# Performance work log

Measured on AMD Instinct MI355X. Metric: run time of the kernel, lower is better.

The kernel has to match this reference:

```python
import jax, jax.numpy as jnp
import numpy as np

N = 4096
M0 = 2048
M1 = 2048
MCS = 4096
STRIDE = 2
D_NNGP = STRIDE ** 2 * M1              # 8192, input dim of layer-1 arccos maps
D_NTK = STRIDE ** 2 * (MCS + M1)       # 24576, input dim1 of layer-1 count sketch


def setup_inputs() -> dict:
    key = jax.random.key(0)
    ks = jax.random.split(key, 8)
    return {
        "layer_idx": 1,
        "z_nngp": jax.random.normal(ks[0], (N, D_NNGP), jnp.float32),
        "z_ntk": jax.random.normal(ks[1], (N, D_NTK), jnp.float32),
        "W0": jax.random.normal(ks[2], (D_NNGP, M0), jnp.float32),   # arccos0[1].W
        "W1": jax.random.normal(ks[3], (D_NNGP, M1), jnp.float32),   # arccos1[1].W
        "sign1": (jax.random.randint(ks[4], (D_NTK,), 0, 2) * 2 - 1).astype(jnp.float32),
        "indx1": jax.random.randint(ks[5], (D_NTK,), 0, MCS),
        "sign2": (jax.random.randint(ks[6], (M0,), 0, 2) * 2 - 1).astype(jnp.float32),
        "indx2": jax.random.randint(ks[7], (M0,), 0, MCS),
    }


def count_sketch(x, indx, sign, out_dim):
    # x: [n, d_in]; sign-multiply then scatter_add along last axis into out_dim bins
    xs = x * sign[None, :]
    out = jnp.zeros((x.shape[0], out_dim), dtype=x.dtype)
    return out.at[:, indx].add(xs)


def reference(layer_idx, z_nngp, z_ntk, W0, W1, sign1, indx1, sign2, indx2):
    norm0 = np.sqrt(2.0 / M0).astype(np.float32)
    norm1 = np.float32(np.sqrt(2.0 / M1) / 2.0)
    # arccos order-0 feature map (step function)
    xw0 = z_nngp @ W0
    tmp = (xw0 > 0).astype(z_nngp.dtype) * norm0          # [N, M0]
    # arccos order-1 feature map (relu-like: |xw| + xw)
    xw1 = z_nngp @ W1
    z_nngp_out = (jnp.abs(xw1) + xw1) * norm1             # [N, M1]
    # tensor sketch: count-sketch both, FFT, complex pointwise multiply, ifft.real
    x_cs = count_sketch(z_ntk, indx1, sign1, MCS)         # [N, MCS]
    y_cs = count_sketch(tmp, indx2, sign2, MCS)           # [N, MCS]
    z_ntk_out = jnp.fft.ifft(jnp.fft.fft(x_cs, axis=-1) * jnp.fft.fft(y_cs, axis=-1)).real
    z_ntk_cat = jnp.concatenate([z_nngp_out, z_ntk_out], axis=1)  # [N, M1+MCS]
    return (z_nngp_out, z_ntk_cat)
```

## Files before the change

kernel.cpp:

```cpp
#include <hip/hip_runtime.h>

#define NROW 4096
#define KDIM 8192
#define MDIM 2048
#define MCS_ 4096
#define DNTK 24576
#define CATW 6144
#define TAU_HALF 2.5e-3f
#define NT (KDIM / 32)

typedef __attribute__((ext_vector_type(8))) short short8;
typedef __attribute__((ext_vector_type(4))) float f32x4;

__device__ __forceinline__ void split2(float x0, float x1,
                                       unsigned& hi, unsigned& lo) {
    const unsigned u0 = __float_as_uint(x0);
    const unsigned u1 = __float_as_uint(x1);
    hi = (u0 >> 16) | (u1 & 0xFFFF0000u);
    const float l0 = x0 - __uint_as_float(u0 & 0xFFFF0000u);
    const float l1 = x1 - __uint_as_float(u1 & 0xFFFF0000u);
    lo = (__float_as_uint(l0) >> 16) | (__float_as_uint(l1) & 0xFFFF0000u);
}

__device__ __forceinline__ float2 cmulf(float2 a, float2 b) {
    return make_float2(a.x * b.x - a.y * b.y, a.x * b.y + a.y * b.x);
}

__global__ __launch_bounds__(512, 2) void gemm_mfma(
    const float* __restrict__ A,
    const float* __restrict__ W1,
    const float* __restrict__ W0,
    float* __restrict__ out0,
    float* __restrict__ outCat)
{
    const int mode = blockIdx.z;
    const float* __restrict__ W = mode ? W0 : W1;

    __shared__ short8 AhiS[2][1024], AloS[2][1024];
    __shared__ short8 BhiS[2][1024], BloS[2][1024];

    const int tid  = threadIdx.x;
    const int lane = tid & 63;
    const int wid  = tid >> 6;
    const int wr   = wid >> 1;
    const int wc   = wid & 1;
    const int brow = blockIdx.y * 256;
    const int bcol = blockIdx.x * 256;

    f32x4 acc[4][8];
#pragma unroll
    for (int m = 0; m < 4; ++m)
#pragma unroll
        for (int n = 0; n < 8; ++n)
#pragma unroll
            for (int i = 0; i < 4; ++i) acc[m][n][i] = 0.f;

    const int srow  = tid >> 1;
    const int skh   = tid & 1;
    const int slot0 = (srow >> 4) * 64 + (srow & 15) + (skh << 5);
    const float* aptr = A + (size_t)(brow + srow) * KDIM + skh * 16;
    const float* bptr = W + (size_t)(skh * 16) * MDIM + (bcol + srow);

    float4 av0, av1, av2, av3;
    float  bst[16];

#define LOAD_TILE(T)                                                         \
    {                                                                        \
        const float* ap = aptr + (T) * 32;                                   \
        av0 = *reinterpret_cast<const float4*>(ap);                          \
        av1 = *reinterpret_cast<const float4*>(ap + 4);                      \
        av2 = *reinterpret_cast<const float4*>(ap + 8);                      \
        av3 = *reinterpret_cast<const float4*>(ap + 12);                     \
        const float* bp = bptr + (size_t)((T) * 32) * MDIM;                  \
        _Pragma("unroll")                                                    \
        for (int j = 0; j < 16; ++j) bst[j] = bp[(size_t)j * MDIM];          \
    }

#define CONVERT_WRITE(BUF)                                                   \
    {                                                                        \
        union { short8 s; unsigned u[4]; } h, l;                             \
        split2(av0.x, av0.y, h.u[0], l.u[0]);                                \
        split2(av0.z, av0.w, h.u[1], l.u[1]);                                \
        split2(av1.x, av1.y, h.u[2], l.u[2]);                                \
        split2(av1.z, av1.w, h.u[3], l.u[3]);                                \
        AhiS[BUF][slot0] = h.s;  AloS[BUF][slot0] = l.s;                     \
        split2(av2.x, av2.y, h.u[0], l.u[0]);                                \
        split2(av2.z, av2.w, h.u[1], l.u[1]);                                \
        split2(av3.x, av3.y, h.u[2], l.u[2]);                                \
        split2(av3.z, av3.w, h.u[3], l.u[3]);                                \
        AhiS[BUF][slot0 + 16] = h.s;  AloS[BUF][slot0 + 16] = l.s;           \
        split2(bst[0], bst[1], h.u[0], l.u[0]);                              \
        split2(bst[2], bst[3], h.u[1], l.u[1]);                              \
        split2(bst[4], bst[5], h.u[2], l.u[2]);                              \
        split2(bst[6], bst[7], h.u[3], l.u[3]);                              \
        BhiS[BUF][slot0] = h.s;  BloS[BUF][slot0] = l.s;                     \
        split2(bst[8],  bst[9],  h.u[0], l.u[0]);                            \
        split2(bst[10], bst[11], h.u[1], l.u[1]);                            \
        split2(bst[12], bst[13], h.u[2], l.u[2]);                            \
        split2(bst[14], bst[15], h.u[3], l.u[3]);                            \
        BhiS[BUF][slot0 + 16] = h.s;  BloS[BUF][slot0 + 16] = l.s;           \
    }

    LOAD_TILE(0);
    CONVERT_WRITE(0);
    LOAD_TILE(1);
    __syncthreads();

    for (int t = 0; t < NT; ++t) {
        const int cur = t & 1;

        short8 ah[4], al[4];
#pragma unroll
        for (int m = 0; m < 4; ++m) {
            ah[m] = AhiS[cur][(wr * 4 + m) * 64 + lane];
            al[m] = AloS[cur][(wr * 4 + m) * 64 + lane];
        }

        if (t + 1 < NT) {
            CONVERT_WRITE(cur ^ 1);
            if (t + 2 < NT) LOAD_TILE(t + 2);
        }

#pragma unroll
        for (int n = 0; n < 8; ++n) {
            const short8 bh = BhiS[cur][(wc * 8 + n) * 64 + lane];
            const short8 bl = BloS[cur][(wc * 8 + n) * 64 + lane];
#pragma unroll
            for (int m = 0; m < 4; ++m) {
                acc[m][n] = __builtin_amdgcn_mfma_f32_16x16x32_bf16(
                    ah[m], bh, acc[m][n], 0, 0, 0);
                acc[m][n] = __builtin_amdgcn_mfma_f32_16x16x32_bf16(
                    ah[m], bl, acc[m][n], 0, 0, 0);
                acc[m][n] = __builtin_amdgcn_mfma_f32_16x16x32_bf16(
                    al[m], bh, acc[m][n], 0, 0, 0);
            }
        }
        __syncthreads();
    }
#undef LOAD_TILE
#undef CONVERT_WRITE

    const float norm0 = 0.03125f;
    const int ocol0 = bcol + wc * 128 + (lane & 15);
    const int orow0 = brow + wr * 64 + ((lane >> 4) << 2);
#pragma unroll
    for (int m = 0; m < 4; ++m)
#pragma unroll
        for (int n = 0; n < 8; ++n) {
            const int col = ocol0 + n * 16;
#pragma unroll
            for (int i = 0; i < 4; ++i) {
                const int row = orow0 + m * 16 + i;
                if (mode == 0) {
                    const float v = fmaxf(acc[m][n][i], 0.f) * norm0;
                    out0[(size_t)row * MDIM + col] = v;
                    outCat[(size_t)row * CATW + col] = v;
                } else {
                    outCat[(size_t)row * CATW + 2048 + col] = acc[m][n][i];
                }
            }
        }
}

__global__ __launch_bounds__(512) void sketch_fft_kernel(
    const float* __restrict__ z_ntk,
    const float* __restrict__ sign1,
    const int*   __restrict__ indx1,
    const float* __restrict__ sign2,
    const int*   __restrict__ indx2,
    float* __restrict__ outCat)
{
    __shared__ float2 Z[MCS_];
    __shared__ float2 RT[1024];
    float* Zf = reinterpret_cast<float*>(Z);
    const int tid = threadIdx.x;
    const int row = blockIdx.x;

    for (int i = tid; i < 2048; i += 512)
        reinterpret_cast<float4*>(Zf)[i] = make_float4(0.f, 0.f, 0.f, 0.f);
    const float wconst = -1.5339807878856412e-3f;
    for (int t = tid; t < 1024; t += 512) {
        float sw, cw;
        __sincosf(wconst * (float)t, &sw, &cw);
        RT[t] = make_float2(cw, sw);
    }
    __syncthreads();

    const float4* xrow4 = reinterpret_cast<const float4*>(z_ntk + (size_t)row * DNTK);
    const float4* s1v   = reinterpret_cast<const float4*>(sign1);
    const int4*   i1v   = reinterpret_cast<const int4*>(indx1);
    for (int v = tid; v < DNTK / 4; v += 512) {
        const float4 x = xrow4[v];
        const float4 s = s1v[v];
        const int4   ix = i1v[v];
        atomicAdd(&Zf[ix.x], x.x * s.x);
        atomicAdd(&Zf[ix.y], x.y * s.y);
        atomicAdd(&Zf[ix.z], x.z * s.z);
        atomicAdd(&Zf[ix.w], x.w * s.w);
    }
    const float norm0 = 0.03125f;
    const float* trow = outCat + (size_t)row * CATW + 2048;
    const float4* t4v = reinterpret_cast<const float4*>(trow);
    const float4* s2v = reinterpret_cast<const float4*>(sign2);
    const int4*   i2v = reinterpret_cast<const int4*>(indx2);
    for (int v = tid; v < MDIM / 4; v += 512) {
        const float4 t4 = t4v[v];
        const float4 s  = s2v[v];
        const int4   ix = i2v[v];
        const float y0 = (fabsf(t4.x) < TAU_HALF) ? 0.5f * norm0 : (t4.x > 0.f ? norm0 : 0.f);
        const float y1 = (fabsf(t4.y) < TAU_HALF) ? 0.5f * norm0 : (t4.y > 0.f ? norm0 : 0.f);
        const float y2 = (fabsf(t4.z) < TAU_HALF) ? 0.5f * norm0 : (t4.z > 0.f ? norm0 : 0.f);
        const float y3 = (fabsf(t4.w) < TAU_HALF) ? 0.5f * norm0 : (t4.w > 0.f ? norm0 : 0.f);
        atomicAdd(&Zf[4096 + ix.x], y0 * s.x);
        atomicAdd(&Zf[4096 + ix.y], y1 * s.y);
        atomicAdd(&Zf[4096 + ix.z], y2 * s.z);
        atomicAdd(&Zf[4096 + ix.w], y3 * s.w);
    }
    __syncthreads();

    {
        float re[8], im[8];
#pragma unroll
        for (int j = 0; j < 8; ++j) {
            const int i = tid + j * 512;
            re[j] = Zf[i];
            im[j] = Zf[4096 + i];
        }
        __syncthreads();
#pragma unroll
        for (int j = 0; j < 8; ++j) {
            const int i = tid + j * 512;
            Z[i] = make_float2(re[j], im[j]);
        }
    }
    __syncthreads();

#pragma unroll
    for (int s = 0; s < 6; ++s) {
        const int lq = 2 * (5 - s);
        const int q  = 1 << lq;
        for (int b = tid; b < 1024; b += 512) {
            const int j    = b & (q - 1);
            const int base = ((b >> lq) << (lq + 2)) + j;
            const float2 x0 = Z[base];
            const float2 x1 = Z[base + q];
            const float2 x2 = Z[base + 2 * q];
            const float2 x3 = Z[base + 3 * q];
            const float2 w1 = RT[j << (10 - lq)];
            const float2 w2 = cmulf(w1, w1);
            const float2 w3 = cmulf(w2, w1);
            const float2 sA = make_float2(x0.x + x2.x, x0.y + x2.y);
            const float2 sB = make_float2(x0.x - x2.x, x0.y - x2.y);
            const float2 sC = make_float2(x1.x + x3.x, x1.y + x3.y);
            const float2 sD = make_float2(x1.x - x3.x, x1.y - x3.y);
            Z[base] = make_float2(sA.x + sC.x, sA.y + sC.y);
            const float2 u1 = make_float2(sB.x + sD.y, sB.y - sD.x);
            const float2 u2 = make_float2(sA.x - sC.x, sA.y - sC.y);
            const float2 u3 = make_float2(sB.x - sD.y, sB.y + sD.x);
            Z[base + q]     = cmulf(u1, w1);
            Z[base + 2 * q] = cmulf(u2, w2);
            Z[base + 3 * q] = cmulf(u3, w3);
        }
        __syncthreads();
    }

    for (int p = tid; p < MCS_; p += 512) {
        int q;
        if (p == 0) q = 0;
        else { const int h = 31 - __clz(p); q = 5 * (1 << (h & ~1)) - 1 - p; }
        if (p <= q) {
            const float2 Ap = Z[p];
            const float2 Bq = Z[q];
            const float Xr = 0.5f * (Ap.x + Bq.x);
            const float Xi = 0.5f * (Ap.y - Bq.y);
            const float Yr = 0.5f * (Ap.y + Bq.y);
            const float Yi = -0.5f * (Ap.x - Bq.x);
            const float Pr = Xr * Yr - Xi * Yi;
            const float Pi = Xr * Yi + Xi * Yr;
            Z[p] = make_float2(Pr, Pi);
            Z[q] = make_float2(Pr, -Pi);
        }
    }
    __syncthreads();

#pragma unroll
    for (int s = 0; s < 6; ++s) {
        const int lq = 2 * s;
        const int q  = 1 << lq;
        for (int b = tid; b < 1024; b += 512) {
            const int j    = b & (q - 1);
            const int base = ((b >> lq) << (lq + 2)) + j;
            const float2 t1 = RT[j << (10 - lq)];
            const float2 w1 = make_float2(t1.x, -t1.y);
            const float2 w2 = cmulf(w1, w1);
            const float2 w3 = cmulf(w2, w1);
            const float2 a  = Z[base];
            const float2 b1 = cmulf(Z[base + q],     w1);
            const float2 c  = cmulf(Z[base + 2 * q], w2);
            const float2 d  = cmulf(Z[base + 3 * q], w3);
            const float2 sA = make_float2(a.x + c.x, a.y + c.y);
            const float2 sB = make_float2(a.x - c.x, a.y - c.y);
            const float2 sC = make_float2(b1.x + d.x, b1.y + d.y);
            const float2 sD = make_float2(b1.x - d.x, b1.y - d.y);
            Z[base]         = make_float2(sA.x + sC.x, sA.y + sC.y);
            Z[base + q]     = make_float2(sB.x - sD.y, sB.y + sD.x);
            Z[base + 2 * q] = make_float2(sA.x - sC.x, sA.y - sC.y);
            Z[base + 3 * q] = make_float2(sB.x + sD.y, sB.y - sD.x);
        }
        __syncthreads();
    }

    float* orow = outCat + (size_t)row * CATW + 2048;
    const float scale = 1.0f / (float)MCS_;
    for (int n = tid; n < MCS_; n += 512) orow[n] = Z[n].x * scale;
}

extern "C" void kernel_launch(void* const* d_in, const int* in_sizes, int n_in,
                              void* d_out, int out_size, void* d_ws, size_t ws_size,
                              hipStream_t stream) {
    (void)in_sizes; (void)n_in; (void)out_size; (void)d_ws; (void)ws_size;
    const float* z_nngp = (const float*)d_in[1];
    const float* z_ntk  = (const float*)d_in[2];
    const float* W0     = (const float*)d_in[3];
    const float* W1     = (const float*)d_in[4];
    const float* sign1  = (const float*)d_in[5];
    const int*   indx1  = (const int*)d_in[6];
    const float* sign2  = (const float*)d_in[7];
    const int*   indx2  = (const int*)d_in[8];

    float* out0   = (float*)d_out;
    float* outCat = out0 + (size_t)NROW * MDIM;

    gemm_mfma<<<dim3(MDIM / 256, NROW / 256, 2), dim3(512), 0, stream>>>(
        z_nngp, W1, W0, out0, outCat);

    sketch_fft_kernel<<<dim3(NROW), dim3(512), 0, stream>>>(
        z_ntk, sign1, indx1, sign2, indx2, outCat);
}
```

Measured before the change: 1.349 ms.

## Pre-split GEMM operands to bf16 hi/lo tiles in workspace; pad FFT shared memory

Adds a conversion kernel that splits A and both W matrices once into bf16 hi/lo pairs, stored in the MFMA tile layout in the workspace. A new GEMM kernel then streams these pre-tiled operands straight into shared memory, so the per-tile fp32 split and the strided column gathers of W disappear from the main loop. The FFT kernel also pads its shared array to avoid bank conflicts, halves the twiddle table by using symmetry, and batches the count-sketch loads ahead of the atomics. The cost is an extra pass over the inputs and 256 MB of workspace; if the workspace is too small the old GEMM path runs instead.

```diff
diff --git a/kernel.cpp b/kernel.cpp
--- a/kernel.cpp
+++ b/kernel.cpp
@@ -24,6 +24,164 @@
 
 __device__ __forceinline__ float2 cmulf(float2 a, float2 b) {
     return make_float2(a.x * b.x - a.y * b.y, a.x * b.y + a.y * b.x);
+}
+
+__global__ __launch_bounds__(512) void convert_kernel(
+    const float* __restrict__ A,
+    const float* __restrict__ W1,
+    const float* __restrict__ W0,
+    short8* __restrict__ aHi, short8* __restrict__ aLo,
+    short8* __restrict__ wHi, short8* __restrict__ wLo)
+{
+    int b = blockIdx.x;
+    const int tid = threadIdx.x;
+    if (b < 4096) {
+        const int P = b >> 8, T = b & 255;
+        const float* src = A + (size_t)(P * 256) * KDIM + T * 32;
+        short8* dh = aHi + ((size_t)b << 10);
+        short8* dl = aLo + ((size_t)b << 10);
+        for (int s = tid; s < 1024; s += 512) {
+            const int row = ((s >> 6) << 4) | (s & 15);
+            const int k0  = ((s >> 4) & 3) * 8;
+            const float* p = src + (size_t)row * KDIM + k0;
+            const float4 v0 = *reinterpret_cast<const float4*>(p);
+            const float4 v1 = *reinterpret_cast<const float4*>(p + 4);
+            union { short8 ss; unsigned u[4]; } h, l;
+            split2(v0.x, v0.y, h.u[0], l.u[0]);
+            split2(v0.z, v0.w, h.u[1], l.u[1]);
+            split2(v1.x, v1.y, h.u[2], l.u[2]);
+            split2(v1.z, v1.w, h.u[3], l.u[3]);
+            dh[s] = h.ss; dl[s] = l.ss;
+        }
+    } else {
+        b -= 4096;
+        const int mat = b >> 11;
+        const int T   = b & 255;
+        const int Pc  = (b >> 8) & 7;
+        const float* Wm = mat ? W0 : W1;
+        const float* src = Wm + (size_t)(T * 32) * MDIM + Pc * 256;
+        short8* dh = wHi + ((size_t)b << 10);
+        short8* dl = wLo + ((size_t)b << 10);
+        for (int s = tid; s < 1024; s += 512) {
+            const int col = ((s >> 6) << 4) | (s & 15);
+            const int k0  = ((s >> 4) & 3) * 8;
+            float v[8];
+#pragma unroll
+            for (int j = 0; j < 8; ++j)
+                v[j] = src[(size_t)(k0 + j) * MDIM + col];
+            union { short8 ss; unsigned u[4]; } h, l;
+            split2(v[0], v[1], h.u[0], l.u[0]);
+            split2(v[2], v[3], h.u[1], l.u[1]);
+            split2(v[4], v[5], h.u[2], l.u[2]);
+            split2(v[6], v[7], h.u[3], l.u[3]);
+            dh[s] = h.ss; dl[s] = l.ss;
+        }
+    }
+}
+
+__global__ __launch_bounds__(512, 2) void gemm_mfma_pre(
+    const short8* __restrict__ aHi, const short8* __restrict__ aLo,
+    const short8* __restrict__ wHi, const short8* __restrict__ wLo,
+    float* __restrict__ out0, float* __restrict__ outCat)
+{
+    const int mode = blockIdx.z;
+    __shared__ short8 AhiS[2][1024], AloS[2][1024];
+    __shared__ short8 BhiS[2][1024], BloS[2][1024];
+
+    const int tid  = threadIdx.x;
+    const int lane = tid & 63;
+    const int wid  = tid >> 6;
+    const int wr   = wid >> 1;
+    const int wc   = wid & 1;
+    const int brow = blockIdx.y * 256;
+    const int bcol = blockIdx.x * 256;
+
+    const size_t aBase = ((size_t)blockIdx.y) << 18;
+    const size_t wBase = ((size_t)(mode * 8 + blockIdx.x)) << 18;
+
+    f32x4 acc[4][8];
+#pragma unroll
+    for (int m = 0; m < 4; ++m)
+#pragma unroll
+        for (int n = 0; n < 8; ++n)
+#pragma unroll
+            for (int i = 0; i < 4; ++i) acc[m][n][i] = 0.f;
+
+    short8 st[8];
+
+#define ISSUE(T)                                                             \
+    {                                                                        \
+        const size_t o = ((size_t)(T)) << 10;                                \
+        st[0] = aHi[aBase + o + tid];  st[1] = aHi[aBase + o + tid + 512];   \
+        st[2] = aLo[aBase + o + tid];  st[3] = aLo[aBase + o + tid + 512];   \
+        st[4] = wHi[wBase + o + tid];  st[5] = wHi[wBase + o + tid + 512];   \
+        st[6] = wLo[wBase + o + tid];  st[7] = wLo[wBase + o + tid + 512];   \
+    }
+#define WRITE(BUF)                                                           \
+    {                                                                        \
+        AhiS[BUF][tid] = st[0];  AhiS[BUF][tid + 512] = st[1];               \
+        AloS[BUF][tid] = st[2];  AloS[BUF][tid + 512] = st[3];               \
+        BhiS[BUF][tid] = st[4];  BhiS[BUF][tid + 512] = st[5];               \
+        BloS[BUF][tid] = st[6];  BloS[BUF][tid + 512] = st[7];               \
+    }
+
+    ISSUE(0); WRITE(0); ISSUE(1);
+    __syncthreads();
+
+    for (int t = 0; t < NT; ++t) {
+        const int cur = t & 1;
+
+        short8 ah[4], al[4];
+#pragma unroll
+        for (int m = 0; m < 4; ++m) {
+            ah[m] = AhiS[cur][(wr * 4 + m) * 64 + lane];
+            al[m] = AloS[cur][(wr * 4 + m) * 64 + lane];
+        }
+
+        if (t + 1 < NT) {
+            WRITE(cur ^ 1);
+            if (t + 2 < NT) ISSUE(t + 2);
+        }
+
+#pragma unroll
+        for (int n = 0; n < 8; ++n) {
+            const short8 bh = BhiS[cur][(wc * 8 + n) * 64 + lane];
+            const short8 bl = BloS[cur][(wc * 8 + n) * 64 + lane];
+#pragma unroll
+            for (int m = 0; m < 4; ++m) {
+                acc[m][n] = __builtin_amdgcn_mfma_f32_16x16x32_bf16(
+                    ah[m], bh, acc[m][n], 0, 0, 0);
+                acc[m][n] = __builtin_amdgcn_mfma_f32_16x16x32_bf16(
+                    ah[m], bl, acc[m][n], 0, 0, 0);
+                acc[m][n] = __builtin_amdgcn_mfma_f32_16x16x32_bf16(
+                    al[m], bh, acc[m][n], 0, 0, 0);
+            }
+        }
+        __syncthreads();
+    }
+#undef ISSUE
+#undef WRITE
+
+    const float norm0 = 0.03125f;
+    const int ocol0 = bcol + wc * 128 + (lane & 15);
+    const int orow0 = brow + wr * 64 + ((lane >> 4) << 2);
+#pragma unroll
+    for (int m = 0; m < 4; ++m)
+#pragma unroll
+        for (int n = 0; n < 8; ++n) {
+            const int col = ocol0 + n * 16;
+#pragma unroll
+            for (int i = 0; i < 4; ++i) {
+                const int row = orow0 + m * 16 + i;
+                if (mode == 0) {
+                    const float v = fmaxf(acc[m][n][i], 0.f) * norm0;
+                    out0[(size_t)row * MDIM + col] = v;
+                    outCat[(size_t)row * CATW + col] = v;
+                } else {
+                    outCat[(size_t)row * CATW + 2048 + col] = acc[m][n][i];
+                }
+            }
+        }
 }
 
 __global__ __launch_bounds__(512, 2) void gemm_mfma(
@@ -75,7 +233,6 @@
         _Pragma("unroll")                                                    \
         for (int j = 0; j < 16; ++j) bst[j] = bp[(size_t)j * MDIM];          \
     }
-
 #define CONVERT_WRITE(BUF)                                                   \
     {                                                                        \
         union { short8 s; unsigned u[4]; } h, l;                             \
@@ -108,19 +265,16 @@
 
     for (int t = 0; t < NT; ++t) {
         const int cur = t & 1;
-
         short8 ah[4], al[4];
 #pragma unroll
         for (int m = 0; m < 4; ++m) {
             ah[m] = AhiS[cur][(wr * 4 + m) * 64 + lane];
             al[m] = AloS[cur][(wr * 4 + m) * 64 + lane];
         }
-
         if (t + 1 < NT) {
             CONVERT_WRITE(cur ^ 1);
             if (t + 2 < NT) LOAD_TILE(t + 2);
         }
-
 #pragma unroll
         for (int n = 0; n < 8; ++n) {
             const short8 bh = BhiS[cur][(wc * 8 + n) * 64 + lane];
@@ -162,6 +316,15 @@
         }
 }
 
+#define ZP(i) Z[(i) + ((i) >> 4)]
+#define YBASE 4608
+
+__device__ __forceinline__ float2 twfetch(const float2* RT, int t) {
+    if (t <= 512) return RT[t];
+    const float2 r = RT[1024 - t];
+    return make_float2(-r.y, -r.x);
+}
+
 __global__ __launch_bounds__(512) void sketch_fft_kernel(
     const float* __restrict__ z_ntk,
     const float* __restrict__ sign1,
@@ -170,16 +333,16 @@
     const int*   __restrict__ indx2,
     float* __restrict__ outCat)
 {
-    __shared__ float2 Z[MCS_];
-    __shared__ float2 RT[1024];
+    __shared__ float2 Z[4352];
+    __shared__ float2 RT[513];
     float* Zf = reinterpret_cast<float*>(Z);
     const int tid = threadIdx.x;
     const int row = blockIdx.x;
 
-    for (int i = tid; i < 2048; i += 512)
+    for (int i = tid; i < 2176; i += 512)
         reinterpret_cast<float4*>(Zf)[i] = make_float4(0.f, 0.f, 0.f, 0.f);
     const float wconst = -1.5339807878856412e-3f;
-    for (int t = tid; t < 1024; t += 512) {
+    for (int t = tid; t <= 512; t += 512) {
         float sw, cw;
         __sincosf(wconst * (float)t, &sw, &cw);
         RT[t] = make_float2(cw, sw);
@@ -189,32 +352,35 @@
     const float4* xrow4 = reinterpret_cast<const float4*>(z_ntk + (size_t)row * DNTK);
     const float4* s1v   = reinterpret_cast<const float4*>(sign1);
     const int4*   i1v   = reinterpret_cast<const int4*>(indx1);
-    for (int v = tid; v < DNTK / 4; v += 512) {
-        const float4 x = xrow4[v];
-        const float4 s = s1v[v];
-        const int4   ix = i1v[v];
-        atomicAdd(&Zf[ix.x], x.x * s.x);
-        atomicAdd(&Zf[ix.y], x.y * s.y);
-        atomicAdd(&Zf[ix.z], x.z * s.z);
-        atomicAdd(&Zf[ix.w], x.w * s.w);
+    for (int c = 0; c < 12; c += 4) {
+        float4 xs[4], ss[4]; int4 iv[4];
+#pragma unroll
+        for (int j = 0; j < 4; ++j) {
+            const int v = tid + (c + j) * 512;
+            xs[j] = xrow4[v]; ss[j] = s1v[v]; iv[j] = i1v[v];
+        }
+#pragma unroll
+        for (int j = 0; j < 4; ++j) {
+            atomicAdd(&Zf[iv[j].x], xs[j].x * ss[j].x);
+            atomicAdd(&Zf[iv[j].y], xs[j].y * ss[j].y);
+            atomicAdd(&Zf[iv[j].z], xs[j].z * ss[j].z);
+            atomicAdd(&Zf[iv[j].w], xs[j].w * ss[j].w);
+        }
     }
     const float norm0 = 0.03125f;
     const float* trow = outCat + (size_t)row * CATW + 2048;
-    const float4* t4v = reinterpret_cast<const float4*>(trow);
-    const float4* s2v = reinterpret_cast<const float4*>(sign2);
-    const int4*   i2v = reinterpret_cast<const int4*>(indx2);
-    for (int v = tid; v < MDIM / 4; v += 512) {
-        const float4 t4 = t4v[v];
-        const float4 s  = s2v[v];
-        const int4   ix = i2v[v];
+    {
+        const float4 t4 = reinterpret_cast<const float4*>(trow)[tid];
+        const float4 s  = reinterpret_cast<const float4*>(sign2)[tid];
+        const int4   ix = reinterpret_cast<const int4*>(indx2)[tid];
         const float y0 = (fabsf(t4.x) < TAU_HALF) ? 0.5f * norm0 : (t4.x > 0.f ? norm0 : 0.f);
         const float y1 = (fabsf(t4.y) < TAU_HALF) ? 0.5f * norm0 : (t4.y > 0.f ? norm0 : 0.f);
         const float y2 = (fabsf(t4.z) < TAU_HALF) ? 0.5f * norm0 : (t4.z > 0.f ? norm0 : 0.f);
         const float y3 = (fabsf(t4.w) < TAU_HALF) ? 0.5f * norm0 : (t4.w > 0.f ? norm0 : 0.f);
-        atomicAdd(&Zf[4096 + ix.x], y0 * s.x);
-        atomicAdd(&Zf[4096 + ix.y], y1 * s.y);
-        atomicAdd(&Zf[4096 + ix.z], y2 * s.z);
-        atomicAdd(&Zf[4096 + ix.w], y3 * s.w);
+        atomicAdd(&Zf[YBASE + ix.x], y0 * s.x);
+        atomicAdd(&Zf[YBASE + ix.y], y1 * s.y);
+        atomicAdd(&Zf[YBASE + ix.z], y2 * s.z);
+        atomicAdd(&Zf[YBASE + ix.w], y3 * s.w);
     }
     __syncthreads();
 
@@ -224,13 +390,13 @@
         for (int j = 0; j < 8; ++j) {
             const int i = tid + j * 512;
             re[j] = Zf[i];
-            im[j] = Zf[4096 + i];
+            im[j] = Zf[YBASE + i];
         }
         __syncthreads();
 #pragma unroll
         for (int j = 0; j < 8; ++j) {
             const int i = tid + j * 512;
-            Z[i] = make_float2(re[j], im[j]);
+            ZP(i) = make_float2(re[j], im[j]);
         }
     }
     __syncthreads();
@@ -242,24 +408,24 @@
         for (int b = tid; b < 1024; b += 512) {
             const int j    = b & (q - 1);
             const int base = ((b >> lq) << (lq + 2)) + j;
-            const float2 x0 = Z[base];
-            const float2 x1 = Z[base + q];
-            const float2 x2 = Z[base + 2 * q];
-            const float2 x3 = Z[base + 3 * q];
-            const float2 w1 = RT[j << (10 - lq)];
+            const float2 x0 = ZP(base);
+            const float2 x1 = ZP(base + q);
+            const float2 x2 = ZP(base + 2 * q);
+            const float2 x3 = ZP(base + 3 * q);
+            const float2 w1 = twfetch(RT, j << (10 - lq));
             const float2 w2 = cmulf(w1, w1);
             const float2 w3 = cmulf(w2, w1);
             const float2 sA = make_float2(x0.x + x2.x, x0.y + x2.y);
             const float2 sB = make_float2(x0.x - x2.x, x0.y - x2.y);
             const float2 sC = make_float2(x1.x + x3.x, x1.y + x3.y);
             const float2 sD = make_float2(x1.x - x3.x, x1.y - x3.y);
-            Z[base] = make_float2(sA.x + sC.x, sA.y + sC.y);
+            ZP(base) = make_float2(sA.x + sC.x, sA.y + sC.y);
             const float2 u1 = make_float2(sB.x + sD.y, sB.y - sD.x);
             const float2 u2 = make_float2(sA.x - sC.x, sA.y - sC.y);
             const float2 u3 = make_float2(sB.x - sD.y, sB.y + sD.x);
-            Z[base + q]     = cmulf(u1, w1);
-            Z[base + 2 * q] = cmulf(u2, w2);
-            Z[base + 3 * q] = cmulf(u3, w3);
+            ZP(base + q)     = cmulf(u1, w1);
+            ZP(base + 2 * q) = cmulf(u2, w2);
+            ZP(base + 3 * q) = cmulf(u3, w3);
         }
         __syncthreads();
     }
@@ -269,16 +435,16 @@
         if (p == 0) q = 0;
         else { const int h = 31 - __clz(p); q = 5 * (1 << (h & ~1)) - 1 - p; }
         if (p <= q) {
-            const float2 Ap = Z[p];
-            const float2 Bq = Z[q];
+            const float2 Ap = ZP(p);
+            const float2 Bq = ZP(q);
             const float Xr = 0.5f * (Ap.x + Bq.x);
             const float Xi = 0.5f * (Ap.y - Bq.y);
             const float Yr = 0.5f * (Ap.y + Bq.y);
             const float Yi = -0.5f * (Ap.x - Bq.x);
             const float Pr = Xr * Yr - Xi * Yi;
             const float Pi = Xr * Yi + Xi * Yr;
-            Z[p] = make_float2(Pr, Pi);
-            Z[q] = make_float2(Pr, -Pi);
+            ZP(p) = make_float2(Pr, Pi);
+            ZP(q) = make_float2(Pr, -Pi);
         }
     }
     __syncthreads();
@@ -290,35 +456,35 @@
         for (int b = tid; b < 1024; b += 512) {
             const int j    = b & (q - 1);
             const int base = ((b >> lq) << (lq + 2)) + j;
-            const float2 t1 = RT[j << (10 - lq)];
+            const float2 t1 = twfetch(RT, j << (10 - lq));
             const float2 w1 = make_float2(t1.x, -t1.y);
             const float2 w2 = cmulf(w1, w1);
             const float2 w3 = cmulf(w2, w1);
-            const float2 a  = Z[base];
-            const float2 b1 = cmulf(Z[base + q],     w1);
-            const float2 c  = cmulf(Z[base + 2 * q], w2);
-            const float2 d  = cmulf(Z[base + 3 * q], w3);
+            const float2 a  = ZP(base);
+            const float2 b1 = cmulf(ZP(base + q),     w1);
+            const float2 c  = cmulf(ZP(base + 2 * q), w2);
+            const float2 d  = cmulf(ZP(base + 3 * q), w3);
             const float2 sA = make_float2(a.x + c.x, a.y + c.y);
             const float2 sB = make_float2(a.x - c.x, a.y - c.y);
             const float2 sC = make_float2(b1.x + d.x, b1.y + d.y);
             const float2 sD = make_float2(b1.x - d.x, b1.y - d.y);
-            Z[base]         = make_float2(sA.x + sC.x, sA.y + sC.y);
-            Z[base + q]     = make_float2(sB.x - sD.y, sB.y + sD.x);
-            Z[base + 2 * q] = make_float2(sA.x - sC.x, sA.y - sC.y);
-            Z[base + 3 * q] = make_float2(sB.x + sD.y, sB.y - sD.x);
+            ZP(base)         = make_float2(sA.x + sC.x, sA.y + sC.y);
+            ZP(base + q)     = make_float2(sB.x - sD.y, sB.y + sD.x);
+            ZP(base + 2 * q) = make_float2(sA.x - sC.x, sA.y - sC.y);
+            ZP(base + 3 * q) = make_float2(sB.x + sD.y, sB.y - sD.x);
         }
         __syncthreads();
     }
 
     float* orow = outCat + (size_t)row * CATW + 2048;
     const float scale = 1.0f / (float)MCS_;
-    for (int n = tid; n < MCS_; n += 512) orow[n] = Z[n].x * scale;
+    for (int n = tid; n < MCS_; n += 512) orow[n] = ZP(n).x * scale;
 }
 
 extern "C" void kernel_launch(void* const* d_in, const int* in_sizes, int n_in,
                               void* d_out, int out_size, void* d_ws, size_t ws_size,
                               hipStream_t stream) {
-    (void)in_sizes; (void)n_in; (void)out_size; (void)d_ws; (void)ws_size;
+    (void)in_sizes; (void)n_in; (void)out_size;
     const float* z_nngp = (const float*)d_in[1];
     const float* z_ntk  = (const float*)d_in[2];
     const float* W0     = (const float*)d_in[3];
@@ -331,8 +497,20 @@
     float* out0   = (float*)d_out;
     float* outCat = out0 + (size_t)NROW * MDIM;
 
-    gemm_mfma<<<dim3(MDIM / 256, NROW / 256, 2), dim3(512), 0, stream>>>(
-        z_nngp, W1, W0, out0, outCat);
+    const size_t NEED = 268435456ull;
+    if (ws_size >= NEED) {
+        short8* aHi = (short8*)d_ws;
+        short8* aLo = aHi + (1ull << 22);
+        short8* wHi = aLo + (1ull << 22);
+        short8* wLo = wHi + (1ull << 22);
+        convert_kernel<<<dim3(8192), dim3(512), 0, stream>>>(
+            z_nngp, W1, W0, aHi, aLo, wHi, wLo);
+        gemm_mfma_pre<<<dim3(8, 16, 2), dim3(512), 0, stream>>>(
+            aHi, aLo, wHi, wLo, out0, outCat);
+    } else {
+        gemm_mfma<<<dim3(8, 16, 2), dim3(512), 0, stream>>>(
+            z_nngp, W1, W0, out0, outCat);
+    }
 
     sketch_fft_kernel<<<dim3(NROW), dim3(512), 0, stream>>>(
         z_ntk, sign1, indx1, sign2, indx2, outCat);
```

Result: faster. 1.291 ms (-4.3%).
